# Kernel optimization log

Measured on AMD Instinct MI355X. Metric: run time of the kernel, lower is better.

The kernel has to match this reference:

```python
import jax, jax.numpy as jnp
import numpy as np

CHANNELS = 256
C_QK = CHANNELS // 8


def setup_inputs() -> dict:
    key = jax.random.key(0)
    ks = jax.random.split(key, 7)
    b, c, h, w = 8, CHANNELS, 64, 64
    x = jax.random.normal(ks[0], (b, c, h, w), dtype=jnp.float32)
    # 1x1 conv weights stored as [out_ch, in_ch]; biases [out_ch]
    s = 1.0 / np.sqrt(c)
    wq = jax.random.uniform(ks[1], (C_QK, c), jnp.float32, -s, s)
    bq = jax.random.uniform(ks[2], (C_QK,), jnp.float32, -s, s)
    wk = jax.random.uniform(ks[3], (C_QK, c), jnp.float32, -s, s)
    bk = jax.random.uniform(ks[4], (C_QK,), jnp.float32, -s, s)
    wv = jax.random.uniform(ks[5], (c, c), jnp.float32, -s, s)
    bv = jax.random.uniform(ks[6], (c,), jnp.float32, -s, s)
    return {"x": x, "wq": wq, "bq": bq, "wk": wk, "bk": bk, "wv": wv, "bv": bv}


def reference(x, wq, bq, wk, bk, wv, bv):
    b, c, h, w = x.shape
    xf = x.reshape(b, c, h * w)  # [b, c, n]
    # 1x1 convs == per-pixel linear projections
    q = jnp.einsum('oc,bcn->bon', wq, xf) + bq[None, :, None]  # [b, c//8, n]
    k = jnp.einsum('oc,bcn->bon', wk, xf) + bk[None, :, None]  # [b, c//8, n]
    v = jnp.einsum('oc,bcn->bon', wv, xf) + bv[None, :, None]  # [b, c, n]
    # attention[i, j] = q_i . k_j  (no scaling, matching the torch code)
    attn = jnp.einsum('bdi,bdj->bij', q, k)  # [b, n, n]
    attn = jax.nn.softmax(attn, axis=-1)
    # out[:, :, i] = sum_j attn[i, j] * v[:, :, j]
    out = jnp.einsum('bij,bcj->bci', attn, v)  # [b, c, n]
    return out.reshape(b, c, h, w)
```

## Files before the change

kernel.cpp:

```cpp
#include <hip/hip_runtime.h>
#include <stdint.h>

#define NB 8
#define NC 256
#define ND 32
#define NN 4096
#define QT 64
#define KT 32
#define NBUF 3

typedef __attribute__((ext_vector_type(8))) short short8;
typedef __attribute__((ext_vector_type(4))) float float4_;

#define MFMA16(a,b,c) __builtin_amdgcn_mfma_f32_16x16x32_bf16((a),(b),(c),0,0,0)

#if __has_builtin(__builtin_amdgcn_exp2f)
#define EXP2(x) __builtin_amdgcn_exp2f(x)
#else
#define EXP2(x) exp2f(x)
#endif
#define L2E 1.44269504088896f
#define SCB (24.0f * L2E)

__device__ __forceinline__ uint16_t f2bf(float f) {
  uint32_t u = __builtin_bit_cast(uint32_t, f);
  u += 0x7fffu + ((u >> 16) & 1u);
  return (uint16_t)(u >> 16);
}
__device__ __forceinline__ float bf2f(uint16_t h) {
  uint32_t u = (uint32_t)h << 16;
  return __builtin_bit_cast(float, u);
}
__device__ __forceinline__ short8 ld8(const uint16_t* p) {
  return *reinterpret_cast<const short8*>(p);
}
__device__ __forceinline__ void async16(const uint16_t* g, uint16_t* l) {
  __builtin_amdgcn_global_load_lds(
      (const __attribute__((address_space(1))) uint32_t*)g,
      (__attribute__((address_space(3))) uint32_t*)l, 16, 0, 0);
}

__global__ __launch_bounds__(256) void k_prep(
    const float* __restrict__ x, const float* __restrict__ wq,
    const float* __restrict__ wk, const float* __restrict__ wv,
    uint16_t* __restrict__ xTh, uint16_t* __restrict__ xTl,
    uint16_t* __restrict__ Wh, uint16_t* __restrict__ Wl, int use_xl)
{
  int bx = blockIdx.x, tid = threadIdx.x;
  if (bx >= 2048) {
    int e = (bx - 2048) * 256 + tid;
    int r = e >> 8;
    float w = (r < 32) ? wq[e] : (r < 64) ? wk[e - 32 * 256] : wv[e - 64 * 256];
    uint16_t h = f2bf(w);
    Wh[e] = h;
    Wl[e] = f2bf(w - bf2f(h));
    return;
  }
  __shared__ uint32_t tile[64][65];
  int b = bx >> 8, t = bx & 255;
  int c0 = (t >> 6) << 6, n0 = (t & 63) << 6;
  const float* xb = x + ((size_t)b * NC + c0) * NN + n0;
  int cc = tid >> 4, nw = (tid & 15) << 2;
  for (int i = 0; i < 4; i++) {
    int c = cc + 16 * i;
    float4_ v = *reinterpret_cast<const float4_*>(xb + (size_t)c * NN + nw);
    for (int u = 0; u < 4; u++) {
      uint16_t h = f2bf(v[u]);
      uint16_t l = f2bf(v[u] - bf2f(h));
      tile[c][nw + u] = (uint32_t)h | ((uint32_t)l << 16);
    }
  }
  __syncthreads();
  int cw = (tid & 15) << 2, nn = tid >> 4;
  for (int i = 0; i < 4; i++) {
    int n = nn + 16 * i;
    uint32_t p0 = tile[cw + 0][n], p1 = tile[cw + 1][n];
    uint32_t p2 = tile[cw + 2][n], p3 = tile[cw + 3][n];
    size_t o = ((size_t)b * NN + n0 + n) * NC + c0 + cw;
    *(uint32_t*)(xTh + o)     = (p0 & 0xffffu) | (p1 << 16);
    *(uint32_t*)(xTh + o + 2) = (p2 & 0xffffu) | (p3 << 16);
    if (use_xl) {
      *(uint32_t*)(xTl + o)     = (p0 >> 16) | (p1 & 0xffff0000u);
      *(uint32_t*)(xTl + o + 2) = (p2 >> 16) | (p3 & 0xffff0000u);
    }
  }
}

__global__ __launch_bounds__(256) void k_qkv(
    const uint16_t* __restrict__ xTh, const uint16_t* __restrict__ xTl,
    const uint16_t* __restrict__ Wh, const uint16_t* __restrict__ Wl,
    const float* __restrict__ bq, const float* __restrict__ bk,
    const float* __restrict__ bv,
    uint16_t* __restrict__ Qh, uint16_t* __restrict__ Ql,
    uint16_t* __restrict__ Kh, uint16_t* __restrict__ Kl,
    uint16_t* __restrict__ V, int use_xl, int use_lo)
{
  int b = blockIdx.x & 7, n0 = (blockIdx.x >> 3) * 64;
  int tid = threadIdx.x, wid = tid >> 6, lane = tid & 63;
  int l15 = lane & 15, quad = lane >> 4;
  int nb = n0 + wid * 16;
  float4_ acc[20];
  for (int m = 0; m < 20; m++) acc[m] = (float4_){0.f, 0.f, 0.f, 0.f};
  for (int ks = 0; ks < 8; ks++) {
    size_t xa = ((size_t)b * NN + nb + l15) * NC + ks * 32 + quad * 8;
    short8 bh = ld8(xTh + xa);
    short8 blo;
    if (use_xl) blo = ld8(xTl + xa);
    for (int mt = 0; mt < 20; mt++) {
      size_t wa = (size_t)(16 * mt + l15) * NC + ks * 32 + quad * 8;
      short8 ah = ld8(Wh + wa);
      acc[mt] = MFMA16(ah, bh, acc[mt]);
      if (mt < 4) {
        short8 al = ld8(Wl + wa);
        acc[mt] = MFMA16(al, bh, acc[mt]);
      }
      if (use_xl) acc[mt] = MFMA16(ah, blo, acc[mt]);
    }
  }
  int n = nb + l15;
  for (int mt = 0; mt < 20; mt++) {
    for (int r = 0; r < 4; r++) {
      int row = 16 * mt + quad * 4 + r;
      float v = acc[mt][r];
      if (mt < 2) {
        v = (v + bq[row]) * L2E;
        size_t o = ((size_t)b * NN + n) * ND + row;
        uint16_t h = f2bf(v);
        Qh[o] = h;
        if (use_lo) Ql[o] = f2bf(v - bf2f(h));
      } else if (mt < 4) {
        int rk = row - 32;
        v += bk[rk];
        size_t o = ((size_t)b * NN + n) * ND + rk;
        uint16_t h = f2bf(v);
        Kh[o] = h;
        if (use_lo) Kl[o] = f2bf(v - bf2f(h));
      } else {
        int c = row - 64;
        v += bv[c];
        V[((size_t)b * NC + c) * NN + n] = f2bf(v);
      }
    }
  }
}

__global__ __launch_bounds__(512) void k_attn(
    const uint16_t* __restrict__ Qh, const uint16_t* __restrict__ Ql,
    const uint16_t* __restrict__ Kh, const uint16_t* __restrict__ Kl,
    const uint16_t* __restrict__ V, float* __restrict__ out, int use_lo)
{
  __shared__ uint16_t sV[NBUF][256][KT];
  __shared__ uint16_t sP[4][16][40];
  __shared__ float sL[QT];

  int bx = blockIdx.x;
  int b = bx & 7;
  int q0 = (bx >> 3) * QT;
  int tid = threadIdx.x, wid = tid >> 6, lane = tid & 63;
  int l15 = lane & 15, quad = lane >> 4;
  const size_t qkb = (size_t)b * NN * ND;
  const uint16_t* Vb = V + (size_t)b * NC * NN;
  const bool heavy = (wid < 4);

  int sw = (l15 >> 1) & 3;
  auto stageV = [&](int j) {
    int buf = j % NBUF;
    int j0 = j * KT;
    for (int i = 0; i < 4; i++) {
      int sl = (wid - 4) * 256 + 64 * i + lane;
      int c = sl >> 2;
      int q2s = (sl & 3) ^ ((sl >> 3) & 3);
      const uint16_t* g = Vb + (size_t)c * NN + j0 + q2s * 8;
      uint16_t* l = &sV[buf][0][0] + ((wid - 4) * 4 + i) * 512;
      async16(g, l);
    }
  };

  float4_ acc[2][4];
  for (int m = 0; m < 2; m++) for (int n = 0; n < 4; n++)
    acc[m][n] = (float4_){0.f, 0.f, 0.f, 0.f};
  float l_part = 0.f;

  short8 qfh, qfl, kh0, kh1, kl0, kl1;
  if (heavy) {
    size_t a = qkb + (size_t)(q0 + wid * 16 + l15) * ND + quad * 8;
    qfh = ld8(Qh + a);
    if (use_lo) qfl = ld8(Ql + a);
    size_t a0 = qkb + (size_t)l15 * ND + quad * 8;
    size_t a1 = qkb + (size_t)(16 + l15) * ND + quad * 8;
    kh0 = ld8(Kh + a0); kh1 = ld8(Kh + a1);
    if (use_lo) { kl0 = ld8(Kl + a0); kl1 = ld8(Kl + a1); }
  } else {
    stageV(0);
    stageV(1);
  }

  for (int j = 0; j < NN / KT; j++) {
    int buf = j % NBUF;
    if (heavy) {
      short8 nh0, nh1, nl0, nl1;
      if (j < NN / KT - 1) {
        size_t a0 = qkb + (size_t)((j + 1) * KT + l15) * ND + quad * 8;
        size_t a1 = a0 + 16 * ND;
        nh0 = ld8(Kh + a0); nh1 = ld8(Kh + a1);
        if (use_lo) { nl0 = ld8(Kl + a0); nl1 = ld8(Kl + a1); }
      }
      float4_ S0 = (float4_){0.f,0.f,0.f,0.f}, S1 = S0;
      S0 = MFMA16(kh0, qfh, S0);
      S1 = MFMA16(kh1, qfh, S1);
      if (use_lo) {
        S0 = MFMA16(kl0, qfh, S0); S0 = MFMA16(kh0, qfl, S0);
        S1 = MFMA16(kl1, qfh, S1); S1 = MFMA16(kh1, qfl, S1);
      }
      float p0[4], p1[4];
      for (int r = 0; r < 4; r++) {
        p0[r] = EXP2(S0[r] - SCB);
        p1[r] = EXP2(S1[r] - SCB);
      }
      l_part += ((p0[0] + p0[1]) + (p0[2] + p0[3])) +
                ((p1[0] + p1[1]) + (p1[2] + p1[3]));
      uint2 w0, w1;
      w0.x = (uint32_t)f2bf(p0[0]) | ((uint32_t)f2bf(p0[1]) << 16);
      w0.y = (uint32_t)f2bf(p0[2]) | ((uint32_t)f2bf(p0[3]) << 16);
      w1.x = (uint32_t)f2bf(p1[0]) | ((uint32_t)f2bf(p1[1]) << 16);
      w1.y = (uint32_t)f2bf(p1[2]) | ((uint32_t)f2bf(p1[3]) << 16);
      *reinterpret_cast<uint2*>(&sP[wid][l15][4 * quad]) = w0;
      *reinterpret_cast<uint2*>(&sP[wid][l15][16 + 4 * quad]) = w1;
      kh0 = nh0; kh1 = nh1;
      if (use_lo) { kl0 = nl0; kl1 = nl1; }
    } else {
      if (j < NN / KT - 2) stageV(j + 2);
    }
    __syncthreads();
    short8 bfP[4];
    for (int qt = 0; qt < 4; qt++)
      bfP[qt] = ld8(&sP[qt][l15][quad * 8]);
    for (int mt = 0; mt < 2; mt++) {
      short8 af = ld8(&sV[buf][wid * 32 + 16 * mt + l15][(quad ^ sw) * 8]);
      for (int qt = 0; qt < 4; qt++)
        acc[mt][qt] = MFMA16(af, bfP[qt], acc[mt][qt]);
    }
    __syncthreads();
  }

  if (heavy) {
    float l_tot = l_part;
    l_tot += __shfl_xor(l_tot, 16);
    l_tot += __shfl_xor(l_tot, 32);
    if (quad == 0) sL[wid * 16 + l15] = l_tot;
  }
  __syncthreads();
  float linv[4];
  for (int qt = 0; qt < 4; qt++) linv[qt] = 1.0f / sL[qt * 16 + l15];
  for (int mt = 0; mt < 2; mt++)
    for (int qt = 0; qt < 4; qt++)
      for (int r = 0; r < 4; r++) {
        int c = wid * 32 + 16 * mt + quad * 4 + r;
        int q = q0 + qt * 16 + l15;
        out[((size_t)(b * NC + c)) * NN + q] = acc[mt][qt][r] * linv[qt];
      }
}

extern "C" void kernel_launch(void* const* d_in, const int* in_sizes, int n_in,
                              void* d_out, int out_size, void* d_ws, size_t ws_size,
                              hipStream_t stream)
{
  const float* x  = (const float*)d_in[0];
  const float* wq = (const float*)d_in[1];
  const float* bq = (const float*)d_in[2];
  const float* wk = (const float*)d_in[3];
  const float* bk = (const float*)d_in[4];
  const float* wv = (const float*)d_in[5];
  const float* bv = (const float*)d_in[6];
  float* out = (float*)d_out;

  const size_t szXT = (size_t)NB * NN * NC * 2;
  const size_t szW  = (size_t)320 * 256 * 2;
  const size_t szQK = (size_t)NB * NN * ND * 2;
  const size_t szV  = (size_t)NB * NC * NN * 2;
  size_t needA = 2 * szXT + 2 * szW + 4 * szQK + szV;
  size_t needB = szXT + 2 * szW + 4 * szQK + szV;
  int use_xl = ws_size >= needA;
  int use_lo = ws_size >= needB;

  char* p = (char*)d_ws;
  uint16_t* xTh = (uint16_t*)p; p += szXT;
  uint16_t* xTl = use_xl ? (uint16_t*)p : xTh; if (use_xl) p += szXT;
  uint16_t* Wh = (uint16_t*)p; p += szW;
  uint16_t* Wl = (uint16_t*)p; p += szW;
  uint16_t* Qh = (uint16_t*)p; p += szQK;
  uint16_t* Ql = use_lo ? (uint16_t*)p : xTh; if (use_lo) p += szQK;
  uint16_t* Kh = (uint16_t*)p; p += szQK;
  uint16_t* Kl = use_lo ? (uint16_t*)p : xTh; if (use_lo) p += szQK;
  uint16_t* Vw = (uint16_t*)p;

  hipLaunchKernelGGL(k_prep, dim3(2368), dim3(256), 0, stream,
                     x, wq, wk, wv, xTh, xTl, Wh, Wl, use_xl);
  hipLaunchKernelGGL(k_qkv, dim3(512), dim3(256), 0, stream,
                     xTh, xTl, Wh, Wl, bq, bk, bv, Qh, Ql, Kh, Kl, Vw,
                     use_xl, use_lo);
  hipLaunchKernelGGL(k_attn, dim3(512), dim3(512), 0, stream,
                     Qh, Ql, Kh, Kl, Vw, out, use_lo);
}
```

Before: 280.5 us.

## Fuse x transpose/bf16 split into projection kernel with LDS-staged weights

Removes the separate prep pass that wrote transposed bf16 hi/lo copies of x to global memory. The projection kernel now reads fp32 x directly, splits it into bf16 hi/lo in shared memory, and streams pre-tiled weight slices through LDS with register prefetch. This avoids roughly 32MB of intermediate global traffic. In exchange it adds extra barriers per k-step, more LDS use, and more weight re-reads across 1024 blocks. It also drops the workspace-size fallbacks and always uses the lo parts.

```diff
diff --git a/kernel.cpp b/kernel.cpp
--- a/kernel.cpp
+++ b/kernel.cpp
@@ -40,104 +40,113 @@
       (__attribute__((address_space(3))) uint32_t*)l, 16, 0, 0);
 }
 
-__global__ __launch_bounds__(256) void k_prep(
-    const float* __restrict__ x, const float* __restrict__ wq,
-    const float* __restrict__ wk, const float* __restrict__ wv,
-    uint16_t* __restrict__ xTh, uint16_t* __restrict__ xTl,
-    uint16_t* __restrict__ Wh, uint16_t* __restrict__ Wl, int use_xl)
+__global__ __launch_bounds__(256) void k_w(
+    const float* __restrict__ wq, const float* __restrict__ wk,
+    const float* __restrict__ wv, uint16_t* __restrict__ Wt)
 {
-  int bx = blockIdx.x, tid = threadIdx.x;
-  if (bx >= 2048) {
-    int e = (bx - 2048) * 256 + tid;
-    int r = e >> 8;
-    float w = (r < 32) ? wq[e] : (r < 64) ? wk[e - 32 * 256] : wv[e - 64 * 256];
-    uint16_t h = f2bf(w);
-    Wh[e] = h;
-    Wl[e] = f2bf(w - bf2f(h));
-    return;
-  }
-  __shared__ uint32_t tile[64][65];
-  int b = bx >> 8, t = bx & 255;
-  int c0 = (t >> 6) << 6, n0 = (t & 63) << 6;
-  const float* xb = x + ((size_t)b * NC + c0) * NN + n0;
-  int cc = tid >> 4, nw = (tid & 15) << 2;
-  for (int i = 0; i < 4; i++) {
-    int c = cc + 16 * i;
-    float4_ v = *reinterpret_cast<const float4_*>(xb + (size_t)c * NN + nw);
-    for (int u = 0; u < 4; u++) {
-      uint16_t h = f2bf(v[u]);
-      uint16_t l = f2bf(v[u] - bf2f(h));
-      tile[c][nw + u] = (uint32_t)h | ((uint32_t)l << 16);
-    }
-  }
-  __syncthreads();
-  int cw = (tid & 15) << 2, nn = tid >> 4;
-  for (int i = 0; i < 4; i++) {
-    int n = nn + 16 * i;
-    uint32_t p0 = tile[cw + 0][n], p1 = tile[cw + 1][n];
-    uint32_t p2 = tile[cw + 2][n], p3 = tile[cw + 3][n];
-    size_t o = ((size_t)b * NN + n0 + n) * NC + c0 + cw;
-    *(uint32_t*)(xTh + o)     = (p0 & 0xffffu) | (p1 << 16);
-    *(uint32_t*)(xTh + o + 2) = (p2 & 0xffffu) | (p3 << 16);
-    if (use_xl) {
-      *(uint32_t*)(xTl + o)     = (p0 >> 16) | (p1 & 0xffff0000u);
-      *(uint32_t*)(xTl + o + 2) = (p2 >> 16) | (p3 & 0xffff0000u);
-    }
-  }
-}
-
-__global__ __launch_bounds__(256) void k_qkv(
-    const uint16_t* __restrict__ xTh, const uint16_t* __restrict__ xTl,
-    const uint16_t* __restrict__ Wh, const uint16_t* __restrict__ Wl,
+  int e = blockIdx.x * 256 + threadIdx.x;
+  int ks = e / 12288, rem = e % 12288;
+  int row = rem >> 5, k32 = rem & 31;
+  int col = ks * 32 + k32;
+  bool lo = row >= 320;
+  int r = lo ? row - 320 : row;
+  float w = (r < 32) ? wq[r * 256 + col]
+          : (r < 64) ? wk[(r - 32) * 256 + col]
+                     : wv[(r - 64) * 256 + col];
+  uint16_t h = f2bf(w);
+  Wt[e] = lo ? f2bf(w - bf2f(h)) : h;
+}
+
+__global__ __launch_bounds__(256) void k_proj(
+    const float* __restrict__ x, const uint16_t* __restrict__ Wt,
     const float* __restrict__ bq, const float* __restrict__ bk,
     const float* __restrict__ bv,
     uint16_t* __restrict__ Qh, uint16_t* __restrict__ Ql,
     uint16_t* __restrict__ Kh, uint16_t* __restrict__ Kl,
-    uint16_t* __restrict__ V, int use_xl, int use_lo)
+    uint16_t* __restrict__ V)
 {
-  int b = blockIdx.x & 7, n0 = (blockIdx.x >> 3) * 64;
-  int tid = threadIdx.x, wid = tid >> 6, lane = tid & 63;
-  int l15 = lane & 15, quad = lane >> 4;
-  int nb = n0 + wid * 16;
-  float4_ acc[20];
-  for (int m = 0; m < 20; m++) acc[m] = (float4_){0.f, 0.f, 0.f, 0.f};
+  __shared__ uint16_t sX[2][32][264];
+  __shared__ uint16_t sW[384 * 40];
+
+  int b = blockIdx.x & 7, n0 = (blockIdx.x >> 3) * 32;
+  int tid = threadIdx.x;
+  const uint4* Wt4 = (const uint4*)Wt;
+
+  uint4 wpre[6];
+  for (int u = 0; u < 6; u++) wpre[u] = Wt4[u * 256 + tid];
+
+  for (int a = 0; a < 4; a++) {
+    int idx = a * 256 + tid;
+    int cp = idx >> 3;
+    int nq = idx & 7;
+    const float* pa = x + ((size_t)(b * NC + 2 * cp)) * NN + n0 + nq * 4;
+    float4_ va = *reinterpret_cast<const float4_*>(pa);
+    float4_ vb = *reinterpret_cast<const float4_*>(pa + NN);
+    for (int i = 0; i < 4; i++) {
+      int n = nq * 4 + i;
+      uint16_t ha = f2bf(va[i]), hb = f2bf(vb[i]);
+      uint16_t la = f2bf(va[i] - bf2f(ha)), lb = f2bf(vb[i] - bf2f(hb));
+      *(uint32_t*)&sX[0][n][2 * cp] = (uint32_t)ha | ((uint32_t)hb << 16);
+      *(uint32_t*)&sX[1][n][2 * cp] = (uint32_t)la | ((uint32_t)lb << 16);
+    }
+  }
+  __syncthreads();
+
+  auto writeW = [&]() {
+    for (int u = 0; u < 6; u++) {
+      int c = u * 256 + tid;
+      int row = c >> 2, q = c & 3;
+      *reinterpret_cast<uint4*>(&sW[row * 40 + q * 8]) = wpre[u];
+    }
+  };
+  writeW();
+  for (int u = 0; u < 6; u++) wpre[u] = Wt4[1536 + u * 256 + tid];
+  __syncthreads();
+
+  int wid = tid >> 6, lane = tid & 63, l15 = lane & 15, quad = lane >> 4;
+  int ng = wid & 1, rh = wid >> 1;
+  float4_ acc[10];
+  for (int m = 0; m < 10; m++) acc[m] = (float4_){0.f, 0.f, 0.f, 0.f};
+
   for (int ks = 0; ks < 8; ks++) {
-    size_t xa = ((size_t)b * NN + nb + l15) * NC + ks * 32 + quad * 8;
-    short8 bh = ld8(xTh + xa);
-    short8 blo;
-    if (use_xl) blo = ld8(xTl + xa);
-    for (int mt = 0; mt < 20; mt++) {
-      size_t wa = (size_t)(16 * mt + l15) * NC + ks * 32 + quad * 8;
-      short8 ah = ld8(Wh + wa);
-      acc[mt] = MFMA16(ah, bh, acc[mt]);
+    short8 bh  = ld8(&sX[0][ng * 16 + l15][ks * 32 + quad * 8]);
+    short8 blo = ld8(&sX[1][ng * 16 + l15][ks * 32 + quad * 8]);
+    for (int mi = 0; mi < 10; mi++) {
+      int mt = rh * 10 + mi;
+      short8 ah = ld8(&sW[(16 * mt + l15) * 40 + quad * 8]);
+      acc[mi] = MFMA16(ah, bh, acc[mi]);
       if (mt < 4) {
-        short8 al = ld8(Wl + wa);
-        acc[mt] = MFMA16(al, bh, acc[mt]);
-      }
-      if (use_xl) acc[mt] = MFMA16(ah, blo, acc[mt]);
-    }
-  }
-  int n = nb + l15;
-  for (int mt = 0; mt < 20; mt++) {
+        short8 al = ld8(&sW[(320 + 16 * mt + l15) * 40 + quad * 8]);
+        acc[mi] = MFMA16(al, bh, acc[mi]);
+      }
+      acc[mi] = MFMA16(ah, blo, acc[mi]);
+    }
+    if (ks < 7) {
+      __syncthreads();
+      writeW();
+      if (ks < 6)
+        for (int u = 0; u < 6; u++)
+          wpre[u] = Wt4[(size_t)(ks + 2) * 1536 + u * 256 + tid];
+      __syncthreads();
+    }
+  }
+
+  int n = n0 + ng * 16 + l15;
+  for (int mi = 0; mi < 10; mi++) {
+    int mt = rh * 10 + mi;
     for (int r = 0; r < 4; r++) {
       int row = 16 * mt + quad * 4 + r;
-      float v = acc[mt][r];
-      if (mt < 2) {
+      float v = acc[mi][r];
+      if (row < 32) {
         v = (v + bq[row]) * L2E;
         size_t o = ((size_t)b * NN + n) * ND + row;
-        uint16_t h = f2bf(v);
-        Qh[o] = h;
-        if (use_lo) Ql[o] = f2bf(v - bf2f(h));
-      } else if (mt < 4) {
-        int rk = row - 32;
-        v += bk[rk];
+        uint16_t h = f2bf(v); Qh[o] = h; Ql[o] = f2bf(v - bf2f(h));
+      } else if (row < 64) {
+        int rk = row - 32; v += bk[rk];
         size_t o = ((size_t)b * NN + n) * ND + rk;
-        uint16_t h = f2bf(v);
-        Kh[o] = h;
-        if (use_lo) Kl[o] = f2bf(v - bf2f(h));
+        uint16_t h = f2bf(v); Kh[o] = h; Kl[o] = f2bf(v - bf2f(h));
       } else {
-        int c = row - 64;
-        v += bv[c];
+        int c = row - 64; v += bv[c];
         V[((size_t)b * NC + c) * NN + n] = f2bf(v);
       }
     }
@@ -274,31 +283,19 @@
   const float* bv = (const float*)d_in[6];
   float* out = (float*)d_out;
 
-  const size_t szXT = (size_t)NB * NN * NC * 2;
-  const size_t szW  = (size_t)320 * 256 * 2;
+  const size_t szWt = (size_t)8 * 384 * 32 * 2;
   const size_t szQK = (size_t)NB * NN * ND * 2;
-  const size_t szV  = (size_t)NB * NC * NN * 2;
-  size_t needA = 2 * szXT + 2 * szW + 4 * szQK + szV;
-  size_t needB = szXT + 2 * szW + 4 * szQK + szV;
-  int use_xl = ws_size >= needA;
-  int use_lo = ws_size >= needB;
-
   char* p = (char*)d_ws;
-  uint16_t* xTh = (uint16_t*)p; p += szXT;
-  uint16_t* xTl = use_xl ? (uint16_t*)p : xTh; if (use_xl) p += szXT;
-  uint16_t* Wh = (uint16_t*)p; p += szW;
-  uint16_t* Wl = (uint16_t*)p; p += szW;
+  uint16_t* Wt = (uint16_t*)p; p += szWt;
   uint16_t* Qh = (uint16_t*)p; p += szQK;
-  uint16_t* Ql = use_lo ? (uint16_t*)p : xTh; if (use_lo) p += szQK;
+  uint16_t* Ql = (uint16_t*)p; p += szQK;
   uint16_t* Kh = (uint16_t*)p; p += szQK;
-  uint16_t* Kl = use_lo ? (uint16_t*)p : xTh; if (use_lo) p += szQK;
+  uint16_t* Kl = (uint16_t*)p; p += szQK;
   uint16_t* Vw = (uint16_t*)p;
 
-  hipLaunchKernelGGL(k_prep, dim3(2368), dim3(256), 0, stream,
-                     x, wq, wk, wv, xTh, xTl, Wh, Wl, use_xl);
-  hipLaunchKernelGGL(k_qkv, dim3(512), dim3(256), 0, stream,
-                     xTh, xTl, Wh, Wl, bq, bk, bv, Qh, Ql, Kh, Kl, Vw,
-                     use_xl, use_lo);
+  hipLaunchKernelGGL(k_w, dim3(384), dim3(256), 0, stream, wq, wk, wv, Wt);
+  hipLaunchKernelGGL(k_proj, dim3(1024), dim3(256), 0, stream,
+                     x, Wt, bq, bk, bv, Qh, Ql, Kh, Kl, Vw);
   hipLaunchKernelGGL(k_attn, dim3(512), dim3(512), 0, stream,
-                     Qh, Ql, Kh, Kl, Vw, out, use_lo);
-}
+                     Qh, Ql, Kh, Kl, Vw, out, 1);
+}
```

Result: slower. 340.9 us (+21.5%).
